# Kernel tuning notes

Measured on AMD Instinct MI355X. Metric: run time of the kernel, lower is better.

## Reference

```python
import jax, jax.numpy as jnp
import numpy as np

N_NODES = 100000
N_EDGES = 3200000
F_IN = 512
HIDDEN = 16
N_CLASSES = 64
EPS = 1e-12  # F.normalize eps


def agnn_layer(x, src, dst, beta, n_nodes):
    """AGNNConv: cosine-similarity attention + segment softmax + scatter aggregate.
    x: [N, H]; src/dst: [E] (messages flow src -> dst, softmax over edges per dst).
    """
    norm = jnp.sqrt(jnp.sum(x * x, axis=-1, keepdims=True))
    xn = x / jnp.maximum(norm, EPS)                      # L2-normalized features
    cos = jnp.sum(xn[src] * xn[dst], axis=-1)            # [E] cosine similarity
    logits = beta * cos
    m = jax.ops.segment_max(logits, dst, num_segments=n_nodes)   # stable softmax per dst
    e = jnp.exp(logits - m[dst])
    denom = jax.ops.segment_sum(e, dst, num_segments=n_nodes)
    alpha = e / denom[dst]                               # [E]
    return jax.ops.segment_sum(alpha[:, None] * x[src], dst, num_segments=n_nodes)


def setup_inputs() -> dict:
    key = jax.random.key(0)
    ks = jax.random.split(key, 6)
    x = jax.random.normal(ks[0], (N_NODES, F_IN), dtype=jnp.float32)
    edge_index = jax.random.randint(ks[1], (2, N_EDGES), 0, N_NODES, dtype=jnp.int64)
    W1 = jax.random.normal(ks[2], (F_IN, HIDDEN), dtype=jnp.float32) * (1.0 / np.sqrt(F_IN))
    b1 = jnp.zeros((HIDDEN,), dtype=jnp.float32)
    W2 = jax.random.normal(ks[3], (HIDDEN, N_CLASSES), dtype=jnp.float32) * (1.0 / np.sqrt(HIDDEN))
    b2 = jnp.zeros((N_CLASSES,), dtype=jnp.float32)
    beta1 = jnp.ones((), dtype=jnp.float32)  # AGNNConv beta init = 1.0
    beta2 = jnp.ones((), dtype=jnp.float32)
    return {"x": x, "edge_index": edge_index, "W1": W1, "b1": b1,
            "W2": W2, "b2": b2, "beta1": beta1, "beta2": beta2}


def reference(x, edge_index, W1, b1, W2, b2, beta1, beta2):
    n = x.shape[0]
    # PyG AGNNConv adds self-loops before propagation
    loops = jnp.arange(n, dtype=edge_index.dtype)
    src = jnp.concatenate([edge_index[0], loops])
    dst = jnp.concatenate([edge_index[1], loops])
    # eval mode: dropout is identity
    h = jax.nn.relu(x @ W1 + b1)                 # [N, 16]
    h = agnn_layer(h, src, dst, beta1, n)
    h = agnn_layer(h, src, dst, beta2, n)
    out = h @ W2 + b2                            # [N, num_classes]
    return jax.nn.log_softmax(out, axis=1)
```

## Files before the change

kernel.cpp:

```cpp
#include <hip/hip_runtime.h>
#include <hip/hip_bf16.h>

#define F_IN 512
#define HID 16
#define NCLS 64
#define NBUCK_MAX 512
#define EPB 8192

__global__ __launch_bounds__(256) void gemm1_kernel(
    const float* __restrict__ x, const float* __restrict__ W1,
    const float* __restrict__ b1, float* __restrict__ h0,
    float* __restrict__ inv0, int N, int totalWaves)
{
    int wid  = (blockIdx.x * blockDim.x + threadIdx.x) >> 6;
    int lane = threadIdx.x & 63;
    float bias = b1[lane & 15];
    bool s3 = (lane & 8) != 0;
    bool s2 = (lane & 4) != 0;
    bool s1 = (lane & 2) != 0;
    bool s0 = (lane & 1) != 0;

    for (int row = wid; row < N; row += totalWaves) {
        const float4* xp = (const float4*)(x + (size_t)row * F_IN + 8 * lane);
        float4 ta = xp[0], tb = xp[1];
        float xv[8] = {ta.x, ta.y, ta.z, ta.w, tb.x, tb.y, tb.z, tb.w};

        float acc[16];
#pragma unroll
        for (int i = 0; i < 16; ++i) acc[i] = 0.f;

#pragma unroll
        for (int kk = 0; kk < 8; ++kk) {
            const float4* wp = (const float4*)(W1 + (size_t)(8 * lane + kk) * HID);
            float xs = xv[kk];
#pragma unroll
            for (int jj = 0; jj < 4; ++jj) {
                float4 t = wp[jj];
                acc[jj * 4 + 0] += xs * t.x;
                acc[jj * 4 + 1] += xs * t.y;
                acc[jj * 4 + 2] += xs * t.z;
                acc[jj * 4 + 3] += xs * t.w;
            }
        }

#pragma unroll
        for (int i = 0; i < 8; ++i) {
            float k = s3 ? acc[i + 8] : acc[i];
            float s = s3 ? acc[i] : acc[i + 8];
            acc[i] = k + __shfl_xor(s, 8);
        }
#pragma unroll
        for (int i = 0; i < 4; ++i) {
            float k = s2 ? acc[i + 4] : acc[i];
            float s = s2 ? acc[i] : acc[i + 4];
            acc[i] = k + __shfl_xor(s, 4);
        }
#pragma unroll
        for (int i = 0; i < 2; ++i) {
            float k = s1 ? acc[i + 2] : acc[i];
            float s = s1 ? acc[i] : acc[i + 2];
            acc[i] = k + __shfl_xor(s, 2);
        }
        {
            float k = s0 ? acc[1] : acc[0];
            float s = s0 ? acc[0] : acc[1];
            acc[0] = k + __shfl_xor(s, 1);
        }
        acc[0] += __shfl_xor(acc[0], 16);
        acc[0] += __shfl_xor(acc[0], 32);

        float val = fmaxf(acc[0] + bias, 0.f);
        if (lane < 16) h0[(size_t)row * HID + lane] = val;

        float q = val * val;
        q += __shfl_xor(q, 1);
        q += __shfl_xor(q, 2);
        q += __shfl_xor(q, 4);
        q += __shfl_xor(q, 8);
        if (lane == 0) inv0[row] = 1.f / fmaxf(sqrtf(q), 1e-12f);
    }
}

__global__ __launch_bounds__(256) void hist1_kernel(
    const int* __restrict__ dst, int E, int EV, int nbuck,
    int* __restrict__ bucketCount)
{
    __shared__ int h[NBUCK_MAX];
    int tid = threadIdx.x;
    for (int j = tid; j < nbuck; j += 256) h[j] = 0;
    __syncthreads();
    int base = blockIdx.x * EPB;
    for (int k = 0; k < EPB / 256; ++k) {
        int i = base + k * 256 + tid;
        if (i < EV) {
            int d = (i < E) ? dst[i] : (i - E);
            atomicAdd(&h[d >> 8], 1);
        }
    }
    __syncthreads();
    for (int j = tid; j < nbuck; j += 256)
        if (h[j]) atomicAdd(&bucketCount[j], h[j]);
}

__global__ __launch_bounds__(512) void bucket_scan_kernel(
    const int* __restrict__ bucketCount, int nbuck,
    int* __restrict__ bucketStart, int* __restrict__ gCursor)
{
    __shared__ int s[512];
    int t = threadIdx.x;
    int v = (t < nbuck) ? bucketCount[t] : 0;
    s[t] = v;
    __syncthreads();
    for (int off = 1; off < 512; off <<= 1) {
        int add = (t >= off) ? s[t - off] : 0;
        __syncthreads();
        s[t] += add;
        __syncthreads();
    }
    int incl = s[t];
    if (t < nbuck) {
        bucketStart[t] = incl - v;
        gCursor[t]     = incl - v;
        if (t == nbuck - 1) bucketStart[nbuck] = incl;
    }
}

__global__ __launch_bounds__(256) void partition_kernel(
    const int* __restrict__ src, const int* __restrict__ dst,
    int E, int EV, int nbuck, int* __restrict__ gCursor,
    unsigned* __restrict__ staged)
{
    __shared__ int h[NBUCK_MAX];
    __shared__ int gb[NBUCK_MAX];
    int tid = threadIdx.x;
    for (int j = tid; j < nbuck; j += 256) h[j] = 0;
    __syncthreads();

    int base = blockIdx.x * EPB;
    for (int k = 0; k < EPB / 256; ++k) {
        int i = base + k * 256 + tid;
        if (i < EV) {
            int d = (i < E) ? dst[i] : (i - E);
            atomicAdd(&h[d >> 8], 1);
        }
    }
    __syncthreads();
    for (int j = tid; j < nbuck; j += 256) {
        int c = h[j];
        if (c) gb[j] = atomicAdd(&gCursor[j], c);
        h[j] = 0;
    }
    __syncthreads();
    for (int k = 0; k < EPB / 256; ++k) {
        int i = base + k * 256 + tid;
        if (i < EV) {
            int s, d;
            if (i < E) { s = src[i]; d = dst[i]; }
            else       { s = i - E;  d = s; }
            int bkt = d >> 8;
            int ofs = atomicAdd(&h[bkt], 1);
            staged[gb[bkt] + ofs] = (unsigned)s | ((unsigned)(d & 255) << 17);
        }
    }
}

__global__ __launch_bounds__(256) void build_csr_kernel(
    const unsigned* __restrict__ staged, const int* __restrict__ bucketStart,
    int* __restrict__ counts, int* __restrict__ rowstart,
    int* __restrict__ esrc, int N)
{
    __shared__ int hist[256];
    __shared__ int s[256];
    __shared__ int cur[256];
    int b   = blockIdx.x;
    int tid = threadIdx.x;
    int start = bucketStart[b];
    int end   = bucketStart[b + 1];

    hist[tid] = 0;
    __syncthreads();
    for (int i = start + tid; i < end; i += 256)
        atomicAdd(&hist[(staged[i] >> 17) & 255], 1);
    __syncthreads();

    int v = hist[tid];
    s[tid] = v;
    __syncthreads();
    for (int off = 1; off < 256; off <<= 1) {
        int add = (tid >= off) ? s[tid - off] : 0;
        __syncthreads();
        s[tid] += add;
        __syncthreads();
    }
    int excl = s[tid] - v;
    int dstg = b * 256 + tid;
    if (dstg < N) {
        counts[dstg]   = v;
        rowstart[dstg] = start + excl;
    }
    cur[tid] = start + excl;
    __syncthreads();

    for (int i = start + tid; i < end; i += 256) {
        unsigned pk = staged[i];
        int dl  = (pk >> 17) & 255;
        int pos = atomicAdd(&cur[dl], 1);
        esrc[pos] = (int)(pk & 0x1FFFFu);
    }
}

__global__ __launch_bounds__(256) void agg_kernel(
    const float* __restrict__ h, const float* __restrict__ inv,
    const int* __restrict__ esrc, const int* __restrict__ rowstart,
    const int* __restrict__ counts, const float* __restrict__ beta_p,
    float* __restrict__ hout, float* __restrict__ invout, int N)
{
    int node = (blockIdx.x * blockDim.x + threadIdx.x) >> 6;
    if (node >= N) return;
    int lane = threadIdx.x & 63;
    int q = lane & 3;
    int e = lane >> 2;

    float beta  = *beta_p;
    float shift = fabsf(beta);
    float4 hd4  = ((const float4*)(h + (size_t)node * HID))[q];
    float  invd = inv[node];
    int start = rowstart[node];
    int cnt   = counts[node];

    float denom = 0.f;
    float4 acc = make_float4(0.f, 0.f, 0.f, 0.f);
    for (int t = e; t < cnt; t += 16) {
        int s = esrc[start + t];
        float4 hs4 = ((const float4*)(h + (size_t)s * HID))[q];
        float invs = inv[s];
        float p = hs4.x * hd4.x + hs4.y * hd4.y + hs4.z * hd4.z + hs4.w * hd4.w;
        p += __shfl_xor(p, 1);
        p += __shfl_xor(p, 2);
        float w = __expf(beta * (p * invd * invs) - shift);
        denom += w;
        acc.x += w * hs4.x;
        acc.y += w * hs4.y;
        acc.z += w * hs4.z;
        acc.w += w * hs4.w;
    }
#pragma unroll
    for (int off = 4; off <= 32; off <<= 1) {
        denom += __shfl_xor(denom, off);
        acc.x += __shfl_xor(acc.x, off);
        acc.y += __shfl_xor(acc.y, off);
        acc.z += __shfl_xor(acc.z, off);
        acc.w += __shfl_xor(acc.w, off);
    }
    float rd = 1.f / denom;
    float4 o = make_float4(acc.x * rd, acc.y * rd, acc.z * rd, acc.w * rd);
    if (lane < 4) ((float4*)(hout + (size_t)node * HID))[q] = o;

    float ss = o.x * o.x + o.y * o.y + o.z * o.z + o.w * o.w;
    ss += __shfl_xor(ss, 1);
    ss += __shfl_xor(ss, 2);
    if (lane == 0) invout[node] = 1.f / fmaxf(sqrtf(ss), 1e-12f);
}

__global__ __launch_bounds__(256) void out_kernel(
    const float* __restrict__ h2, const float* __restrict__ W2,
    const float* __restrict__ b2, float* __restrict__ out, int N)
{
    int wave = (blockIdx.x * blockDim.x + threadIdx.x) >> 6;
    int lane = threadIdx.x & 63;
    if (wave >= N) return;

    float hv = (lane < HID) ? h2[(size_t)wave * HID + lane] : 0.f;
    float acc = b2[lane];
#pragma unroll
    for (int k = 0; k < HID; ++k) {
        float hk = __shfl(hv, k);
        acc += hk * W2[k * NCLS + lane];
    }
    float m = acc;
    for (int off = 32; off > 0; off >>= 1) m = fmaxf(m, __shfl_xor(m, off));
    float e = __expf(acc - m);
    float ssum = e;
    for (int off = 32; off > 0; off >>= 1) ssum += __shfl_xor(ssum, off);
    out[(size_t)wave * NCLS + lane] = (acc - m) - __logf(ssum);
}

extern "C" void kernel_launch(void* const* d_in, const int* in_sizes, int n_in,
                              void* d_out, int out_size, void* d_ws, size_t ws_size,
                              hipStream_t stream)
{
    const float* x     = (const float*)d_in[0];
    const int*   eidx  = (const int*)d_in[1];
    const float* W1    = (const float*)d_in[2];
    const float* b1    = (const float*)d_in[3];
    const float* W2    = (const float*)d_in[4];
    const float* b2    = (const float*)d_in[5];
    const float* beta1 = (const float*)d_in[6];
    const float* beta2 = (const float*)d_in[7];

    int N = in_sizes[0] / F_IN;
    int E = in_sizes[1] / 2;
    const int* src = eidx;
    const int* dst = eidx + E;
    float* out = (float*)d_out;

    int EV    = E + N;
    int nbuck = (N + 255) / 256;

    char* wptr = (char*)d_ws;
    auto alloc = [&](size_t bytes) -> char* {
        char* p = wptr;
        wptr += (bytes + 255) / 256 * 256;
        return p;
    };
    float*    h0       = (float*)alloc((size_t)N * HID * 4);
    float*    inv0     = (float*)alloc((size_t)N * 4);
    float*    h1       = (float*)alloc((size_t)N * HID * 4);
    float*    inv1     = (float*)alloc((size_t)N * 4);
    float*    h2       = (float*)alloc((size_t)N * HID * 4);
    float*    inv2     = (float*)alloc((size_t)N * 4);
    int*      counts   = (int*)alloc((size_t)N * 4);
    int*      rowstart = (int*)alloc((size_t)(N + 1) * 4);
    int*      esrc     = (int*)alloc((size_t)EV * 4);
    unsigned* staged   = (unsigned*)alloc((size_t)EV * 4);
    int*      bucketCount = (int*)alloc((size_t)(nbuck + 1) * 4);
    int*      bucketStart = (int*)alloc((size_t)(nbuck + 1) * 4);
    int*      gCursor     = (int*)alloc((size_t)nbuck * 4);

    int ebBlocks = (EV + EPB - 1) / EPB;

    hipMemsetAsync(bucketCount, 0, (size_t)nbuck * 4, stream);
    hist1_kernel<<<ebBlocks, 256, 0, stream>>>(dst, E, EV, nbuck, bucketCount);
    bucket_scan_kernel<<<1, 512, 0, stream>>>(bucketCount, nbuck, bucketStart, gCursor);
    partition_kernel<<<ebBlocks, 256, 0, stream>>>(src, dst, E, EV, nbuck, gCursor, staged);
    build_csr_kernel<<<nbuck, 256, 0, stream>>>(staged, bucketStart, counts, rowstart,
                                                esrc, N);

    int g1blocks = 2048;
    gemm1_kernel<<<g1blocks, 256, 0, stream>>>(x, W1, b1, h0, inv0, N, g1blocks * 4);

    int aggBlocks = (N + 3) / 4;
    agg_kernel<<<aggBlocks, 256, 0, stream>>>(h0, inv0, esrc, rowstart, counts, beta1,
                                              h1, inv1, N);
    agg_kernel<<<aggBlocks, 256, 0, stream>>>(h1, inv1, esrc, rowstart, counts, beta2,
                                              h2, inv2, N);

    out_kernel<<<(N * 64 + 255) / 256, 256, 0, stream>>>(h2, W2, b2, out, N);
}
```

Measured before the change: 575.2 us.

## Overlap GEMM1 with CSR partition/build kernels and batch rows and edge loads

Removes the standalone GEMM1 launch and splits its rows across extra blocks added to the partition and CSR-build kernels, so the dense x@W1 work runs alongside the memory-bound graph preprocessing. Each GEMM wave now handles four rows per iteration, reusing each W1 load across four rows. The aggregation kernel issues its first four edge gathers up front to expose more memory-level parallelism. In exchange, register pressure rises and the mixed-role kernels rely on a hand-tuned row split between the two launches.

```diff
diff --git a/kernel.cpp b/kernel.cpp
--- a/kernel.cpp
+++ b/kernel.cpp
@@ -7,77 +7,108 @@
 #define NBUCK_MAX 512
 #define EPB 8192
 
-__global__ __launch_bounds__(256) void gemm1_kernel(
+__device__ __forceinline__ void gemm_rows(
     const float* __restrict__ x, const float* __restrict__ W1,
     const float* __restrict__ b1, float* __restrict__ h0,
-    float* __restrict__ inv0, int N, int totalWaves)
-{
-    int wid  = (blockIdx.x * blockDim.x + threadIdx.x) >> 6;
-    int lane = threadIdx.x & 63;
+    float* __restrict__ inv0, int rB, int rE, int wid, int totalWaves, int lane)
+{
     float bias = b1[lane & 15];
-    bool s3 = (lane & 8) != 0;
-    bool s2 = (lane & 4) != 0;
-    bool s1 = (lane & 2) != 0;
-    bool s0 = (lane & 1) != 0;
-
-    for (int row = wid; row < N; row += totalWaves) {
-        const float4* xp = (const float4*)(x + (size_t)row * F_IN + 8 * lane);
-        float4 ta = xp[0], tb = xp[1];
-        float xv[8] = {ta.x, ta.y, ta.z, ta.w, tb.x, tb.y, tb.z, tb.w};
-
-        float acc[16];
-#pragma unroll
-        for (int i = 0; i < 16; ++i) acc[i] = 0.f;
+    const bool s3 = (lane & 8) != 0;
+    const bool s2 = (lane & 4) != 0;
+    const bool s1 = (lane & 2) != 0;
+    const bool s0 = (lane & 1) != 0;
+
+    for (int g = rB + wid * 4; g < rE; g += totalWaves * 4) {
+        int r0 = g;
+        int r1 = (g + 1 < rE) ? g + 1 : rE - 1;
+        int r2 = (g + 2 < rE) ? g + 2 : rE - 1;
+        int r3 = (g + 3 < rE) ? g + 3 : rE - 1;
+
+        float xv[4][8];
+        {
+            const float4* xp0 = (const float4*)(x + (size_t)r0 * F_IN + 8 * lane);
+            const float4* xp1 = (const float4*)(x + (size_t)r1 * F_IN + 8 * lane);
+            const float4* xp2 = (const float4*)(x + (size_t)r2 * F_IN + 8 * lane);
+            const float4* xp3 = (const float4*)(x + (size_t)r3 * F_IN + 8 * lane);
+            float4 a, b;
+            a = xp0[0]; b = xp0[1];
+            xv[0][0]=a.x; xv[0][1]=a.y; xv[0][2]=a.z; xv[0][3]=a.w;
+            xv[0][4]=b.x; xv[0][5]=b.y; xv[0][6]=b.z; xv[0][7]=b.w;
+            a = xp1[0]; b = xp1[1];
+            xv[1][0]=a.x; xv[1][1]=a.y; xv[1][2]=a.z; xv[1][3]=a.w;
+            xv[1][4]=b.x; xv[1][5]=b.y; xv[1][6]=b.z; xv[1][7]=b.w;
+            a = xp2[0]; b = xp2[1];
+            xv[2][0]=a.x; xv[2][1]=a.y; xv[2][2]=a.z; xv[2][3]=a.w;
+            xv[2][4]=b.x; xv[2][5]=b.y; xv[2][6]=b.z; xv[2][7]=b.w;
+            a = xp3[0]; b = xp3[1];
+            xv[3][0]=a.x; xv[3][1]=a.y; xv[3][2]=a.z; xv[3][3]=a.w;
+            xv[3][4]=b.x; xv[3][5]=b.y; xv[3][6]=b.z; xv[3][7]=b.w;
+        }
+
+        float acc[4][16];
+#pragma unroll
+        for (int i = 0; i < 4; ++i)
+#pragma unroll
+            for (int j = 0; j < 16; ++j) acc[i][j] = 0.f;
 
 #pragma unroll
         for (int kk = 0; kk < 8; ++kk) {
             const float4* wp = (const float4*)(W1 + (size_t)(8 * lane + kk) * HID);
-            float xs = xv[kk];
 #pragma unroll
             for (int jj = 0; jj < 4; ++jj) {
                 float4 t = wp[jj];
-                acc[jj * 4 + 0] += xs * t.x;
-                acc[jj * 4 + 1] += xs * t.y;
-                acc[jj * 4 + 2] += xs * t.z;
-                acc[jj * 4 + 3] += xs * t.w;
+#pragma unroll
+                for (int i = 0; i < 4; ++i) {
+                    float xs = xv[i][kk];
+                    acc[i][jj * 4 + 0] += xs * t.x;
+                    acc[i][jj * 4 + 1] += xs * t.y;
+                    acc[i][jj * 4 + 2] += xs * t.z;
+                    acc[i][jj * 4 + 3] += xs * t.w;
+                }
             }
         }
 
-#pragma unroll
-        for (int i = 0; i < 8; ++i) {
-            float k = s3 ? acc[i + 8] : acc[i];
-            float s = s3 ? acc[i] : acc[i + 8];
-            acc[i] = k + __shfl_xor(s, 8);
-        }
+        int rr[4] = {r0, r1, r2, r3};
 #pragma unroll
         for (int i = 0; i < 4; ++i) {
-            float k = s2 ? acc[i + 4] : acc[i];
-            float s = s2 ? acc[i] : acc[i + 4];
-            acc[i] = k + __shfl_xor(s, 4);
-        }
-#pragma unroll
-        for (int i = 0; i < 2; ++i) {
-            float k = s1 ? acc[i + 2] : acc[i];
-            float s = s1 ? acc[i] : acc[i + 2];
-            acc[i] = k + __shfl_xor(s, 2);
-        }
-        {
-            float k = s0 ? acc[1] : acc[0];
-            float s = s0 ? acc[0] : acc[1];
-            acc[0] = k + __shfl_xor(s, 1);
-        }
-        acc[0] += __shfl_xor(acc[0], 16);
-        acc[0] += __shfl_xor(acc[0], 32);
-
-        float val = fmaxf(acc[0] + bias, 0.f);
-        if (lane < 16) h0[(size_t)row * HID + lane] = val;
-
-        float q = val * val;
-        q += __shfl_xor(q, 1);
-        q += __shfl_xor(q, 2);
-        q += __shfl_xor(q, 4);
-        q += __shfl_xor(q, 8);
-        if (lane == 0) inv0[row] = 1.f / fmaxf(sqrtf(q), 1e-12f);
+            float* a = acc[i];
+#pragma unroll
+            for (int u = 0; u < 8; ++u) {
+                float k = s3 ? a[u + 8] : a[u];
+                float s = s3 ? a[u] : a[u + 8];
+                a[u] = k + __shfl_xor(s, 8);
+            }
+#pragma unroll
+            for (int u = 0; u < 4; ++u) {
+                float k = s2 ? a[u + 4] : a[u];
+                float s = s2 ? a[u] : a[u + 4];
+                a[u] = k + __shfl_xor(s, 4);
+            }
+#pragma unroll
+            for (int u = 0; u < 2; ++u) {
+                float k = s1 ? a[u + 2] : a[u];
+                float s = s1 ? a[u] : a[u + 2];
+                a[u] = k + __shfl_xor(s, 2);
+            }
+            {
+                float k = s0 ? a[1] : a[0];
+                float s = s0 ? a[0] : a[1];
+                a[0] = k + __shfl_xor(s, 1);
+            }
+            a[0] += __shfl_xor(a[0], 16);
+            a[0] += __shfl_xor(a[0], 32);
+
+            float val = fmaxf(a[0] + bias, 0.f);
+            bool live = (g + i < rE);
+            if (live && lane < 16) h0[(size_t)rr[i] * HID + lane] = val;
+
+            float qq = val * val;
+            qq += __shfl_xor(qq, 1);
+            qq += __shfl_xor(qq, 2);
+            qq += __shfl_xor(qq, 4);
+            qq += __shfl_xor(qq, 8);
+            if (live && lane == 0) inv0[rr[i]] = 1.f / fmaxf(sqrtf(qq), 1e-12f);
+        }
     }
 }
 
@@ -125,14 +156,24 @@
     }
 }
 
-__global__ __launch_bounds__(256) void partition_kernel(
+__global__ __launch_bounds__(256) void part_gemm_kernel(
     const int* __restrict__ src, const int* __restrict__ dst,
     int E, int EV, int nbuck, int* __restrict__ gCursor,
-    unsigned* __restrict__ staged)
+    unsigned* __restrict__ staged,
+    const float* __restrict__ x, const float* __restrict__ W1,
+    const float* __restrict__ b1, float* __restrict__ h0,
+    float* __restrict__ inv0, int rB, int rE, int csrBlocks, int gemmWaves)
 {
     __shared__ int h[NBUCK_MAX];
     __shared__ int gb[NBUCK_MAX];
     int tid = threadIdx.x;
+
+    if ((int)blockIdx.x >= csrBlocks) {
+        int wid = (((int)blockIdx.x - csrBlocks) * 256 + tid) >> 6;
+        gemm_rows(x, W1, b1, h0, inv0, rB, rE, wid, gemmWaves, tid & 63);
+        return;
+    }
+
     for (int j = tid; j < nbuck; j += 256) h[j] = 0;
     __syncthreads();
 
@@ -164,16 +205,26 @@
     }
 }
 
-__global__ __launch_bounds__(256) void build_csr_kernel(
+__global__ __launch_bounds__(256) void build_gemm_kernel(
     const unsigned* __restrict__ staged, const int* __restrict__ bucketStart,
     int* __restrict__ counts, int* __restrict__ rowstart,
-    int* __restrict__ esrc, int N)
+    int* __restrict__ esrc, int N,
+    const float* __restrict__ x, const float* __restrict__ W1,
+    const float* __restrict__ b1, float* __restrict__ h0,
+    float* __restrict__ inv0, int rB, int rE, int csrBlocks, int gemmWaves)
 {
     __shared__ int hist[256];
     __shared__ int s[256];
     __shared__ int cur[256];
+    int tid = threadIdx.x;
+
+    if ((int)blockIdx.x >= csrBlocks) {
+        int wid = (((int)blockIdx.x - csrBlocks) * 256 + tid) >> 6;
+        gemm_rows(x, W1, b1, h0, inv0, rB, rE, wid, gemmWaves, tid & 63);
+        return;
+    }
+
     int b   = blockIdx.x;
-    int tid = threadIdx.x;
     int start = bucketStart[b];
     int end   = bucketStart[b + 1];
 
@@ -228,12 +279,42 @@
     int start = rowstart[node];
     int cnt   = counts[node];
 
+    int t0 = e, t1 = e + 16, t2 = e + 32, t3 = e + 48;
+    int s0 = esrc[start + (t0 < cnt ? t0 : 0)];
+    int s1 = esrc[start + (t1 < cnt ? t1 : 0)];
+    int s2 = esrc[start + (t2 < cnt ? t2 : 0)];
+    int s3 = esrc[start + (t3 < cnt ? t3 : 0)];
+    const float4* hp = (const float4*)h;
+    float4 a0 = hp[(size_t)s0 * 4 + q];
+    float4 a1 = hp[(size_t)s1 * 4 + q];
+    float4 a2 = hp[(size_t)s2 * 4 + q];
+    float4 a3 = hp[(size_t)s3 * 4 + q];
+    float i0 = inv[s0], i1 = inv[s1], i2 = inv[s2], i3 = inv[s3];
+
     float denom = 0.f;
     float4 acc = make_float4(0.f, 0.f, 0.f, 0.f);
-    for (int t = e; t < cnt; t += 16) {
-        int s = esrc[start + t];
-        float4 hs4 = ((const float4*)(h + (size_t)s * HID))[q];
-        float invs = inv[s];
+
+#define AGG_SLOT(aa, ii, tt)                                                  \
+    {                                                                         \
+        float p = aa.x * hd4.x + aa.y * hd4.y + aa.z * hd4.z + aa.w * hd4.w;  \
+        p += __shfl_xor(p, 1);                                                \
+        p += __shfl_xor(p, 2);                                                \
+        float w = __expf(beta * (p * invd * ii) - shift);                     \
+        w = (tt < cnt) ? w : 0.f;                                             \
+        denom += w;                                                           \
+        acc.x += w * aa.x; acc.y += w * aa.y;                                 \
+        acc.z += w * aa.z; acc.w += w * aa.w;                                 \
+    }
+    AGG_SLOT(a0, i0, t0)
+    AGG_SLOT(a1, i1, t1)
+    AGG_SLOT(a2, i2, t2)
+    AGG_SLOT(a3, i3, t3)
+#undef AGG_SLOT
+
+    for (int t = e + 64; t < cnt; t += 16) {
+        int sr = esrc[start + t];
+        float4 hs4 = hp[(size_t)sr * 4 + q];
+        float invs = inv[sr];
         float p = hs4.x * hd4.x + hs4.y * hd4.y + hs4.z * hd4.z + hs4.w * hd4.w;
         p += __shfl_xor(p, 1);
         p += __shfl_xor(p, 2);
@@ -244,6 +325,7 @@
         acc.z += w * hs4.z;
         acc.w += w * hs4.w;
     }
+
 #pragma unroll
     for (int off = 4; off <= 32; off <<= 1) {
         denom += __shfl_xor(denom, off);
@@ -332,12 +414,16 @@
     hipMemsetAsync(bucketCount, 0, (size_t)nbuck * 4, stream);
     hist1_kernel<<<ebBlocks, 256, 0, stream>>>(dst, E, EV, nbuck, bucketCount);
     bucket_scan_kernel<<<1, 512, 0, stream>>>(bucketCount, nbuck, bucketStart, gCursor);
-    partition_kernel<<<ebBlocks, 256, 0, stream>>>(src, dst, E, EV, nbuck, gCursor, staged);
-    build_csr_kernel<<<nbuck, 256, 0, stream>>>(staged, bucketStart, counts, rowstart,
-                                                esrc, N);
-
-    int g1blocks = 2048;
-    gemm1_kernel<<<g1blocks, 256, 0, stream>>>(x, W1, b1, h0, inv0, N, g1blocks * 4);
+
+    int rSplit   = 60000;
+    int gcBlocks = 1024;
+    int gdBlocks = 768;
+    part_gemm_kernel<<<ebBlocks + gcBlocks, 256, 0, stream>>>(
+        src, dst, E, EV, nbuck, gCursor, staged,
+        x, W1, b1, h0, inv0, 0, rSplit, ebBlocks, gcBlocks * 4);
+    build_gemm_kernel<<<nbuck + gdBlocks, 256, 0, stream>>>(
+        staged, bucketStart, counts, rowstart, esrc, N,
+        x, W1, b1, h0, inv0, rSplit, N, nbuck, gdBlocks * 4);
 
     int aggBlocks = (N + 3) / 4;
     agg_kernel<<<aggBlocks, 256, 0, stream>>>(h0, inv0, esrc, rowstart, counts, beta1,
```

After: 552.5 us. -3.9%, faster.
